# Kernel tuning notes

Measured on AMD Instinct MI355X. Metric: run time of the kernel, lower is better.

Reference implementation:

```python
import jax, jax.numpy as jnp
import numpy as np

N, F_DIM, H_DIM = 8192, 128, 128

def setup_inputs() -> dict:
    key = jax.random.key(0)
    ks = jax.random.split(key, 7)
    inp = {
        "input": jax.random.normal(ks[0], (N, F_DIM), dtype=jnp.float32),
        "wavelets": jax.random.normal(ks[1], (N, N), dtype=jnp.float32) / np.sqrt(N),
        "wavelets_inv": jax.random.normal(ks[2], (N, N), dtype=jnp.float32) / np.sqrt(N),
        # layer 1 params
        "W1": jax.random.uniform(ks[3], (F_DIM, H_DIM), dtype=jnp.float32,
                                 minval=-np.sqrt(6.0/(F_DIM+H_DIM)), maxval=np.sqrt(6.0/(F_DIM+H_DIM))),
        "f1": jax.random.uniform(ks[4], (N,), dtype=jnp.float32, minval=0.9, maxval=1.1),
        # layer 2 params
        "W2": jax.random.uniform(ks[5], (H_DIM, H_DIM), dtype=jnp.float32,
                                 minval=-np.sqrt(6.0/(H_DIM+H_DIM)), maxval=np.sqrt(6.0/(H_DIM+H_DIM))),
        "f2": jax.random.uniform(ks[6], (N,), dtype=jnp.float32, minval=0.9, maxval=1.1),
    }
    return inp

def _gwnn_layer(features, wavelets, wavelets_inv, W, filt):
    # torch: wavelets @ diag(filt) @ (wavelets_inv @ (features @ W))
    # diag(filt) matmul == column-wise scale of wavelets (broadcast elementwise)
    xw = features @ W                      # [N, out]
    spec = wavelets_inv @ xw               # [N, out] spectral-domain features
    spec = filt[:, None] * spec            # apply learnable diagonal filter
    return wavelets @ spec                 # [N, out]

def reference(input, wavelets, wavelets_inv, W1, f1, W2, f2):
    # eval mode: dropout is identity
    h1 = jax.nn.relu(_gwnn_layer(input, wavelets, wavelets_inv, W1, f1))
    out = _gwnn_layer(h1, wavelets, wavelets_inv, W2, f2)
    return out
```

## Files before the change

kernel.cpp:

```cpp
#include <hip/hip_runtime.h>
#include <hip/hip_bf16.h>
#include <stdint.h>


typedef __attribute__((ext_vector_type(4))) float f32x4;
typedef __attribute__((ext_vector_type(8))) short s16x8;
typedef __attribute__((ext_vector_type(4))) short s16x4;

#define DEVI static __device__ __forceinline__

DEVI short bf1(float x){ __bf16 h = (__bf16)x; return __builtin_bit_cast(short, h); }

DEVI s16x8 cvt8(f32x4 lo, f32x4 hi){
  s16x8 r;
#pragma unroll
  for (int i = 0; i < 4; ++i){ r[i] = bf1(lo[i]); r[4+i] = bf1(hi[i]); }
  return r;
}

DEVI void glds16(const void* g, void* l){
  __builtin_amdgcn_global_load_lds((const __attribute__((address_space(1))) void*)g,
                                   (__attribute__((address_space(3))) void*)l, 16, 0, 0);
}

template<int N> DEVI void waitvm(){
  if constexpr (N == 0)       asm volatile("s_waitcnt vmcnt(0)"  ::: "memory");
  else if constexpr (N == 5)  asm volatile("s_waitcnt vmcnt(5)"  ::: "memory");
  else if constexpr (N == 6)  asm volatile("s_waitcnt vmcnt(6)"  ::: "memory");
  else if constexpr (N == 12) asm volatile("s_waitcnt vmcnt(12)" ::: "memory");
  else if constexpr (N == 18) asm volatile("s_waitcnt vmcnt(18)" ::: "memory");
}

__global__ __launch_bounds__(256, 1) void gemm_big(
    const float* __restrict__ Ap, const short* __restrict__ Btp,
    float* __restrict__ Pp, int K, int M)
{
  constexpr int BM = 128, BK = 32;
  constexpr int ASZ = BM*BK*4;
  constexpr int BSZ = 128*BK*2;
  constexpr int TSZ = ASZ + BSZ;
  constexpr int NBUF = 6, PRE = 4;
  __shared__ uint8_t lds[NBUF*TSZ];

  const int tid  = threadIdx.x;
  const int lane = tid & 63;
  const int wv   = tid >> 6;
  const int la   = lane & 15;
  const int g4   = lane >> 4;
  const int bxl  = ((blockIdx.x & 7) << 3) + (blockIdx.x >> 3);
  const int m0   = bxl * BM;
  const int kq   = blockIdx.y;
  const int K4   = K >> 2;
  const int kb   = kq * K4;

  const float* gAbase = Ap + (size_t)m0*K + kb;
  int aoffg[4];
#pragma unroll
  for (int j = 0; j < 4; ++j){
    const int rl = (wv<<5) + (j<<3) + (lane>>3);
    aoffg[j] = rl*K + (((lane&7) ^ (rl&7))<<2);
  }

  const int nb0 = (wv<<5) + (lane>>2);
  const short* gB0 = Btp + (size_t)(nb0    )*K + kb + (((lane&3)^(nb0&3))<<3);
  const short* gB1 = Btp + (size_t)(nb0+16 )*K + kb + (((lane&3)^(nb0&3))<<3);

  int aoff[2][2];
#pragma unroll
  for (int mi = 0; mi < 2; ++mi){
    const int r = (wv<<5) + mi*16 + la;
#pragma unroll
    for (int p = 0; p < 2; ++p)
      aoff[mi][p] = r*128 + ((((g4<<1)+p)^(r&7))<<4);
  }
  int boff[8];
#pragma unroll
  for (int ni = 0; ni < 8; ++ni){
    const int n = ni*16 + la;
    boff[ni] = n*64 + ((g4^(n&3))<<4);
  }

  f32x4 acc[2][8] = {};

  int kk = 0;
  uint8_t* const lend = lds + NBUF*TSZ;
  uint8_t* bs = lds;
  uint8_t* bc = lds;

  auto STAGE = [&](){
    uint8_t* Ab = bs;
    uint8_t* Bb = bs + ASZ;
#pragma unroll
    for (int j = 0; j < 4; ++j)
      glds16(gAbase + aoffg[j] + kk, Ab + (wv<<12) + (j<<10));
    kk += BK;
    glds16(gB0, Bb + (wv<<11));
    glds16(gB1, Bb + (wv<<11) + 1024);
    gB0 += BK; gB1 += BK;
    bs += TSZ; if (bs == lend) bs = lds;
  };

  auto COMPUTE = [&](){
    const uint8_t* Ab = bc;
    const uint8_t* Bb = bc + ASZ;
    s16x8 a0 = cvt8(*(const f32x4*)(Ab + aoff[0][0]),
                    *(const f32x4*)(Ab + aoff[0][1]));
    s16x8 a1 = cvt8(*(const f32x4*)(Ab + aoff[1][0]),
                    *(const f32x4*)(Ab + aoff[1][1]));
#pragma unroll
    for (int ni = 0; ni < 8; ++ni){
      s16x8 b = *(const s16x8*)(Bb + boff[ni]);
      acc[0][ni] = __builtin_amdgcn_mfma_f32_16x16x32_bf16(a0, b, acc[0][ni], 0, 0, 0);
      acc[1][ni] = __builtin_amdgcn_mfma_f32_16x16x32_bf16(a1, b, acc[1][ni], 0, 0, 0);
    }
    bc += TSZ; if (bc == lend) bc = lds;
  };

  const int ns = K4 >> 5;
  for (int s = 0; s < PRE && s < ns; ++s) STAGE();

  for (int t = 0; t < ns; ++t){
    const int ahead = ns - 1 - t;
    if (ahead >= 3)      waitvm<18>();
    else if (ahead == 2) waitvm<12>();
    else if (ahead == 1) waitvm<6>();
    else                 waitvm<0>();
    __builtin_amdgcn_s_barrier();
    asm volatile("" ::: "memory");
    if (t + PRE < ns) STAGE();
    COMPUTE();
    asm volatile("" ::: "memory");
  }

  float* P = Pp + (size_t)kq * M * 128;
  const int rbase = m0 + (wv<<5) + (g4<<2);
#pragma unroll
  for (int mi = 0; mi < 2; ++mi)
#pragma unroll
    for (int ni = 0; ni < 8; ++ni)
#pragma unroll
      for (int r = 0; r < 4; ++r)
        P[(size_t)(rbase + mi*16 + r)*128 + ni*16 + la] = acc[mi][ni][r];
}

template<bool ABF>
__global__ __launch_bounds__(256, 1) void sgemm(
    const void* __restrict__ Ap, const short* __restrict__ Btp,
    void* __restrict__ Outp, int K, int M)
{
  constexpr int BM = 32, BN = 128, BK = 64;
  constexpr int ASZ = ABF ? BM*BK*2 : BM*BK*4;
  constexpr int BSZ = BN*BK*2;
  constexpr int TSZ = ASZ + BSZ;
  constexpr int NL  = ABF ? 5 : 6;
  constexpr int NBUF = 3, PRE = 2;
  __shared__ uint8_t lds[NBUF*TSZ];

  const int tid  = threadIdx.x;
  const int lane = tid & 63;
  const int wv   = tid >> 6;
  const int la   = lane & 15;
  const int g4   = lane >> 4;
  const int m0   = blockIdx.x * BM;

  const float* gA0 = nullptr; const float* gA1 = nullptr; const short* gAh = nullptr;
  if constexpr (!ABF){
    const float* Af = (const float*)Ap;
    int r0 = (wv<<3) + (lane>>4);
    int r1 = r0 + 4;
    gA0 = Af + (size_t)(m0+r0)*K + (((lane&15)^(r0&15))<<2);
    gA1 = Af + (size_t)(m0+r1)*K + (((lane&15)^(r1&15))<<2);
  } else {
    const short* Ah = (const short*)Ap;
    int r = (wv<<3) + (lane>>3);
    gAh = Ah + (size_t)(m0+r)*K + (((lane&7)^(r&7))<<3);
  }
  const int nb0 = (wv<<5) + (lane>>3);
  const short* gB0 = Btp + (size_t)(nb0    )*K + (((lane&7)^(nb0&7))<<3);
  const short* gB1 = Btp + (size_t)(nb0+ 8 )*K + (((lane&7)^(nb0&7))<<3);
  const short* gB2 = Btp + (size_t)(nb0+16 )*K + (((lane&7)^(nb0&7))<<3);
  const short* gB3 = Btp + (size_t)(nb0+24 )*K + (((lane&7)^(nb0&7))<<3);

  int aoff[2][2][2];
  int boff[2][2];
#pragma unroll
  for (int mi = 0; mi < 2; ++mi){
    const int r = mi*16 + la;
#pragma unroll
    for (int kf = 0; kf < 2; ++kf){
      if constexpr (!ABF){
        const int v0 = kf*8 + (g4<<1);
        aoff[mi][kf][0] = r*256 + (((v0  )^(r&15))<<4);
        aoff[mi][kf][1] = r*256 + (((v0+1)^(r&15))<<4);
      } else {
        const int u = kf*4 + g4;
        aoff[mi][kf][0] = r*128 + ((u^(r&7))<<4);
        aoff[mi][kf][1] = 0;
      }
    }
  }
#pragma unroll
  for (int ni = 0; ni < 2; ++ni){
    const int n = (wv<<5) + ni*16 + la;
#pragma unroll
    for (int kf = 0; kf < 2; ++kf){
      const int u = kf*4 + g4;
      boff[ni][kf] = n*128 + ((u^(n&7))<<4);
    }
  }

  f32x4 acc[2][2] = {};

  auto STAGE = [&](uint8_t* buf){
    uint8_t* Ab = buf;
    uint8_t* Bb = buf + ASZ;
    if constexpr (!ABF){
      glds16(gA0, Ab + (wv<<11));
      glds16(gA1, Ab + (wv<<11) + 1024);
      gA0 += BK; gA1 += BK;
    } else {
      glds16(gAh, Ab + (wv<<10));
      gAh += BK;
    }
    glds16(gB0, Bb + (wv<<12));
    glds16(gB1, Bb + (wv<<12) + 1024);
    glds16(gB2, Bb + (wv<<12) + 2048);
    glds16(gB3, Bb + (wv<<12) + 3072);
    gB0 += BK; gB1 += BK; gB2 += BK; gB3 += BK;
  };

  auto COMPUTE = [&](const uint8_t* buf){
    const uint8_t* Ab = buf;
    const uint8_t* Bb = buf + ASZ;
#pragma unroll
    for (int kf = 0; kf < 2; ++kf){
      s16x8 a0, a1, b0, b1;
      if constexpr (!ABF){
        a0 = cvt8(*(const f32x4*)(Ab + aoff[0][kf][0]), *(const f32x4*)(Ab + aoff[0][kf][1]));
        a1 = cvt8(*(const f32x4*)(Ab + aoff[1][kf][0]), *(const f32x4*)(Ab + aoff[1][kf][1]));
      } else {
        a0 = *(const s16x8*)(Ab + aoff[0][kf][0]);
        a1 = *(const s16x8*)(Ab + aoff[1][kf][0]);
      }
      b0 = *(const s16x8*)(Bb + boff[0][kf]);
      b1 = *(const s16x8*)(Bb + boff[1][kf]);
      acc[0][0] = __builtin_amdgcn_mfma_f32_16x16x32_bf16(a0, b0, acc[0][0], 0, 0, 0);
      acc[0][1] = __builtin_amdgcn_mfma_f32_16x16x32_bf16(a0, b1, acc[0][1], 0, 0, 0);
      acc[1][0] = __builtin_amdgcn_mfma_f32_16x16x32_bf16(a1, b0, acc[1][0], 0, 0, 0);
      acc[1][1] = __builtin_amdgcn_mfma_f32_16x16x32_bf16(a1, b1, acc[1][1], 0, 0, 0);
    }
  };

  const int ns = K >> 6;
  uint8_t* const lend = lds + NBUF*TSZ;
  uint8_t* bs = lds;
  uint8_t* bc = lds;
  for (int s = 0; s < PRE && s < ns; ++s){
    STAGE(bs);
    bs += TSZ; if (bs == lend) bs = lds;
  }
  for (int t = 0; t < ns; ++t){
    if (t < ns - 1) waitvm<NL>(); else waitvm<0>();
    __builtin_amdgcn_s_barrier();
    asm volatile("" ::: "memory");
    if (t + PRE < ns){
      STAGE(bs);
      bs += TSZ; if (bs == lend) bs = lds;
    }
    COMPUTE(bc);
    bc += TSZ; if (bc == lend) bc = lds;
    asm volatile("" ::: "memory");
  }

  const int mbase = m0 + (g4<<2);
  const int nc0   = (wv<<5) + la;
#pragma unroll
  for (int mi = 0; mi < 2; ++mi){
#pragma unroll
    for (int ni = 0; ni < 2; ++ni){
      s16x4 pk;
#pragma unroll
      for (int r = 0; r < 4; ++r) pk[r] = bf1(acc[mi][ni][r]);
      *(s16x4*)((short*)Outp + (size_t)(nc0 + (ni<<4))*M + (mbase + (mi<<4))) = pk;
    }
  }
}


__global__ __launch_bounds__(256) void red_t(
    const float* __restrict__ Pp, const float* __restrict__ fp,
    short* __restrict__ out, int M)
{
  __shared__ short t[128*65];
  const size_t S = (size_t)M*128;
  const int m0 = blockIdx.x * 64;
  const int tid = threadIdx.x;
#pragma unroll
  for (int it = 0; it < 8; ++it){
    const int idx = it*256 + tid;
    const int m = idx >> 5, nq = idx & 31;
    const float* base = Pp + (size_t)(m0+m)*128;
    f32x4 a = ((const f32x4*)(base      ))[nq];
    f32x4 b = ((const f32x4*)(base +   S))[nq];
    f32x4 c = ((const f32x4*)(base + 2*S))[nq];
    f32x4 d = ((const f32x4*)(base + 3*S))[nq];
    const float fv = fp[m0+m];
#pragma unroll
    for (int j = 0; j < 4; ++j)
      t[(nq*4+j)*65 + m] = bf1(fv * ((a[j] + b[j]) + (c[j] + d[j])));
  }
  __syncthreads();
#pragma unroll
  for (int it = 0; it < 8; ++it){
    const int idx = it*256 + tid;
    const int n = idx >> 4, mc = idx & 15;
    s16x4 v;
#pragma unroll
    for (int j = 0; j < 4; ++j) v[j] = t[n*65 + mc*4 + j];
    *(s16x4*)(out + (size_t)n*M + m0 + mc*4) = v;
  }
}

__global__ __launch_bounds__(256) void red_r(
    const float* __restrict__ Pp, short* __restrict__ out, int M)
{
  const size_t S = (size_t)M*128;
  const size_t i0 = (size_t)(blockIdx.x*256 + threadIdx.x) * 8;
  s16x8 v;
#pragma unroll
  for (int h = 0; h < 2; ++h){
    f32x4 a = *(const f32x4*)(Pp + i0 + 4*h);
    f32x4 b = *(const f32x4*)(Pp + i0 + 4*h + S);
    f32x4 c = *(const f32x4*)(Pp + i0 + 4*h + 2*S);
    f32x4 d = *(const f32x4*)(Pp + i0 + 4*h + 3*S);
#pragma unroll
    for (int j = 0; j < 4; ++j)
      v[4*h+j] = bf1(fmaxf((a[j] + b[j]) + (c[j] + d[j]), 0.0f));
  }
  *(s16x8*)(out + i0) = v;
}

__global__ __launch_bounds__(256) void red_f(
    const float* __restrict__ Pp, float* __restrict__ out, int M)
{
  const size_t S = (size_t)M*128;
  const size_t i0 = (size_t)(blockIdx.x*256 + threadIdx.x) * 4;
  f32x4 a = *(const f32x4*)(Pp + i0);
  f32x4 b = *(const f32x4*)(Pp + i0 + S);
  f32x4 c = *(const f32x4*)(Pp + i0 + 2*S);
  f32x4 d = *(const f32x4*)(Pp + i0 + 3*S);
  *(f32x4*)(out + i0) = (a + b) + (c + d);
}

__global__ void wtrans_k(const float* __restrict__ W1, const float* __restrict__ W2,
                         short* __restrict__ T1, short* __restrict__ T2){
  const int idx = blockIdx.x*256 + threadIdx.x;
  const int m = idx >> 14, rem = idx & 16383;
  const int n = rem >> 7, k = rem & 127;
  const float* W = m ? W2 : W1;
  short* T = m ? T2 : T1;
  T[n*128 + k] = bf1(W[k*128 + n]);
}

extern "C" void kernel_launch(void* const* d_in, const int* in_sizes, int n_in,
                              void* d_out, int out_size, void* d_ws, size_t ws_size,
                              hipStream_t stream){
  const float* input = (const float*)d_in[0];
  const float* wav   = (const float*)d_in[1];
  const float* winv  = (const float*)d_in[2];
  const float* W1    = (const float*)d_in[3];
  const float* f1    = (const float*)d_in[4];
  const float* W2    = (const float*)d_in[5];
  const float* f2    = (const float*)d_in[6];

  constexpr int M = 8192;
  uint8_t* ws = (uint8_t*)d_ws;
  short* W1T = (short*)(ws);
  short* W2T = (short*)(ws + (32<<10));
  short* XWT = (short*)(ws + (64<<10));
  short* SPT = (short*)(ws + (64<<10) + (2<<20));
  short* H1  = (short*)(ws + (64<<10) + (4<<20));
  float* P   = (float*)(ws + (64<<10) + (6<<20));

  dim3 b(256);
  dim3 gbig(M/128, 4);
  dim3 gns(M/32);
  dim3 grt(M/64);
  dim3 grr(M*128/(256*8));
  dim3 grf(M*128/(256*4));
  dim3 gt(128);

  wtrans_k<<<gt, b, 0, stream>>>(W1, W2, W1T, W2T);
  sgemm<false><<<gns, b, 0, stream>>>(input, W1T, XWT, 128, M);
  gemm_big<<<gbig, b, 0, stream>>>(winv, XWT, P, M, M);
  red_t  <<<grt, b, 0, stream>>>(P, f1, SPT, M);
  gemm_big<<<gbig, b, 0, stream>>>(wav, SPT, P, M, M);
  red_r  <<<grr, b, 0, stream>>>(P, H1, M);
  sgemm<true ><<<gns, b, 0, stream>>>(H1, W2T, XWT, 128, M);
  gemm_big<<<gbig, b, 0, stream>>>(winv, XWT, P, M, M);
  red_t  <<<grt, b, 0, stream>>>(P, f2, SPT, M);
  gemm_big<<<gbig, b, 0, stream>>>(wav, SPT, P, M, M);
  red_f  <<<grf, b, 0, stream>>>(P, (float*)d_out, M);
}
```

Before: 299.2 us.

## Double big-GEMM row tile to 256 and split K eightfold

The main N×N GEMM now uses 256-row tiles (4 m-subtiles per wave), so each loaded B tile feeds twice as many MFMAs. To keep the grid size, K is split 8 ways instead of 4, and the reduction kernels now sum 8 partial buffers. The LDS pipeline shrinks from 6 buffers to 3 with prefetch depth 2 to fit the larger tile. The costs are twice the partial-sum traffic in the reduction kernels and more accumulator registers, and the shallower prefetch may expose more memory latency.

```diff
diff --git a/kernel.cpp b/kernel.cpp
--- a/kernel.cpp
+++ b/kernel.cpp
@@ -27,19 +27,18 @@
   if constexpr (N == 0)       asm volatile("s_waitcnt vmcnt(0)"  ::: "memory");
   else if constexpr (N == 5)  asm volatile("s_waitcnt vmcnt(5)"  ::: "memory");
   else if constexpr (N == 6)  asm volatile("s_waitcnt vmcnt(6)"  ::: "memory");
-  else if constexpr (N == 12) asm volatile("s_waitcnt vmcnt(12)" ::: "memory");
-  else if constexpr (N == 18) asm volatile("s_waitcnt vmcnt(18)" ::: "memory");
+  else if constexpr (N == 10) asm volatile("s_waitcnt vmcnt(10)" ::: "memory");
 }
 
 __global__ __launch_bounds__(256, 1) void gemm_big(
     const float* __restrict__ Ap, const short* __restrict__ Btp,
     float* __restrict__ Pp, int K, int M)
 {
-  constexpr int BM = 128, BK = 32;
+  constexpr int BM = 256, BK = 32;
   constexpr int ASZ = BM*BK*4;
   constexpr int BSZ = 128*BK*2;
   constexpr int TSZ = ASZ + BSZ;
-  constexpr int NBUF = 6, PRE = 4;
+  constexpr int NBUF = 3, PRE = 2;
   __shared__ uint8_t lds[NBUF*TSZ];
 
   const int tid  = threadIdx.x;
@@ -47,17 +46,17 @@
   const int wv   = tid >> 6;
   const int la   = lane & 15;
   const int g4   = lane >> 4;
-  const int bxl  = ((blockIdx.x & 7) << 3) + (blockIdx.x >> 3);
+  const int bxl  = ((blockIdx.x & 7) << 2) + (blockIdx.x >> 3);
   const int m0   = bxl * BM;
   const int kq   = blockIdx.y;
-  const int K4   = K >> 2;
-  const int kb   = kq * K4;
+  const int K8   = K >> 3;
+  const int kb   = kq * K8;
 
   const float* gAbase = Ap + (size_t)m0*K + kb;
-  int aoffg[4];
-#pragma unroll
-  for (int j = 0; j < 4; ++j){
-    const int rl = (wv<<5) + (j<<3) + (lane>>3);
+  int aoffg[8];
+#pragma unroll
+  for (int j = 0; j < 8; ++j){
+    const int rl = (wv<<6) + (j<<3) + (lane>>3);
     aoffg[j] = rl*K + (((lane&7) ^ (rl&7))<<2);
   }
 
@@ -65,22 +64,22 @@
   const short* gB0 = Btp + (size_t)(nb0    )*K + kb + (((lane&3)^(nb0&3))<<3);
   const short* gB1 = Btp + (size_t)(nb0+16 )*K + kb + (((lane&3)^(nb0&3))<<3);
 
-  int aoff[2][2];
-#pragma unroll
-  for (int mi = 0; mi < 2; ++mi){
-    const int r = (wv<<5) + mi*16 + la;
+  int aoff[4][2];
+#pragma unroll
+  for (int mi = 0; mi < 4; ++mi){
+    const int r = (wv<<6) + mi*16 + la;
 #pragma unroll
     for (int p = 0; p < 2; ++p)
-      aoff[mi][p] = r*128 + ((((g4<<1)+p)^(r&7))<<4);
+      aoff[mi][p] = r*128 + ((((g4<<1)+p) ^ (r&7))<<4);
   }
   int boff[8];
 #pragma unroll
   for (int ni = 0; ni < 8; ++ni){
     const int n = ni*16 + la;
-    boff[ni] = n*64 + ((g4^(n&3))<<4);
-  }
-
-  f32x4 acc[2][8] = {};
+    boff[ni] = n*64 + ((g4 ^ (n&3))<<4);
+  }
+
+  f32x4 acc[4][8] = {};
 
   int kk = 0;
   uint8_t* const lend = lds + NBUF*TSZ;
@@ -91,40 +90,39 @@
     uint8_t* Ab = bs;
     uint8_t* Bb = bs + ASZ;
 #pragma unroll
-    for (int j = 0; j < 4; ++j)
-      glds16(gAbase + aoffg[j] + kk, Ab + (wv<<12) + (j<<10));
-    kk += BK;
+    for (int j = 0; j < 8; ++j)
+      glds16(gAbase + aoffg[j] + kk, Ab + (wv<<13) + (j<<10));
     glds16(gB0, Bb + (wv<<11));
     glds16(gB1, Bb + (wv<<11) + 1024);
     gB0 += BK; gB1 += BK;
+    kk += BK;
     bs += TSZ; if (bs == lend) bs = lds;
   };
 
   auto COMPUTE = [&](){
     const uint8_t* Ab = bc;
     const uint8_t* Bb = bc + ASZ;
-    s16x8 a0 = cvt8(*(const f32x4*)(Ab + aoff[0][0]),
-                    *(const f32x4*)(Ab + aoff[0][1]));
-    s16x8 a1 = cvt8(*(const f32x4*)(Ab + aoff[1][0]),
-                    *(const f32x4*)(Ab + aoff[1][1]));
+    s16x8 a0 = cvt8(*(const f32x4*)(Ab + aoff[0][0]), *(const f32x4*)(Ab + aoff[0][1]));
+    s16x8 a1 = cvt8(*(const f32x4*)(Ab + aoff[1][0]), *(const f32x4*)(Ab + aoff[1][1]));
+    s16x8 a2 = cvt8(*(const f32x4*)(Ab + aoff[2][0]), *(const f32x4*)(Ab + aoff[2][1]));
+    s16x8 a3 = cvt8(*(const f32x4*)(Ab + aoff[3][0]), *(const f32x4*)(Ab + aoff[3][1]));
 #pragma unroll
     for (int ni = 0; ni < 8; ++ni){
       s16x8 b = *(const s16x8*)(Bb + boff[ni]);
       acc[0][ni] = __builtin_amdgcn_mfma_f32_16x16x32_bf16(a0, b, acc[0][ni], 0, 0, 0);
       acc[1][ni] = __builtin_amdgcn_mfma_f32_16x16x32_bf16(a1, b, acc[1][ni], 0, 0, 0);
+      acc[2][ni] = __builtin_amdgcn_mfma_f32_16x16x32_bf16(a2, b, acc[2][ni], 0, 0, 0);
+      acc[3][ni] = __builtin_amdgcn_mfma_f32_16x16x32_bf16(a3, b, acc[3][ni], 0, 0, 0);
     }
     bc += TSZ; if (bc == lend) bc = lds;
   };
 
-  const int ns = K4 >> 5;
+  const int ns = K8 >> 5;
   for (int s = 0; s < PRE && s < ns; ++s) STAGE();
 
   for (int t = 0; t < ns; ++t){
-    const int ahead = ns - 1 - t;
-    if (ahead >= 3)      waitvm<18>();
-    else if (ahead == 2) waitvm<12>();
-    else if (ahead == 1) waitvm<6>();
-    else                 waitvm<0>();
+    if (t < ns - 1) waitvm<10>();
+    else            waitvm<0>();
     __builtin_amdgcn_s_barrier();
     asm volatile("" ::: "memory");
     if (t + PRE < ns) STAGE();
@@ -133,9 +131,9 @@
   }
 
   float* P = Pp + (size_t)kq * M * 128;
-  const int rbase = m0 + (wv<<5) + (g4<<2);
-#pragma unroll
-  for (int mi = 0; mi < 2; ++mi)
+  const int rbase = m0 + (wv<<6) + (g4<<2);
+#pragma unroll
+  for (int mi = 0; mi < 4; ++mi)
 #pragma unroll
     for (int ni = 0; ni < 8; ++ni)
 #pragma unroll
@@ -287,6 +285,14 @@
 }
 
 
+DEVI f32x4 sum8(const float* p, size_t S){
+  f32x4 v = (*(const f32x4*)(p)       + *(const f32x4*)(p +   S))
+          + (*(const f32x4*)(p + 2*S) + *(const f32x4*)(p + 3*S));
+  f32x4 w = (*(const f32x4*)(p + 4*S) + *(const f32x4*)(p + 5*S))
+          + (*(const f32x4*)(p + 6*S) + *(const f32x4*)(p + 7*S));
+  return v + w;
+}
+
 __global__ __launch_bounds__(256) void red_t(
     const float* __restrict__ Pp, const float* __restrict__ fp,
     short* __restrict__ out, int M)
@@ -299,15 +305,11 @@
   for (int it = 0; it < 8; ++it){
     const int idx = it*256 + tid;
     const int m = idx >> 5, nq = idx & 31;
-    const float* base = Pp + (size_t)(m0+m)*128;
-    f32x4 a = ((const f32x4*)(base      ))[nq];
-    f32x4 b = ((const f32x4*)(base +   S))[nq];
-    f32x4 c = ((const f32x4*)(base + 2*S))[nq];
-    f32x4 d = ((const f32x4*)(base + 3*S))[nq];
+    f32x4 v = sum8(Pp + (size_t)(m0+m)*128 + nq*4, S);
     const float fv = fp[m0+m];
 #pragma unroll
     for (int j = 0; j < 4; ++j)
-      t[(nq*4+j)*65 + m] = bf1(fv * ((a[j] + b[j]) + (c[j] + d[j])));
+      t[(nq*4+j)*65 + m] = bf1(fv * v[j]);
   }
   __syncthreads();
 #pragma unroll
@@ -329,13 +331,10 @@
   s16x8 v;
 #pragma unroll
   for (int h = 0; h < 2; ++h){
-    f32x4 a = *(const f32x4*)(Pp + i0 + 4*h);
-    f32x4 b = *(const f32x4*)(Pp + i0 + 4*h + S);
-    f32x4 c = *(const f32x4*)(Pp + i0 + 4*h + 2*S);
-    f32x4 d = *(const f32x4*)(Pp + i0 + 4*h + 3*S);
+    f32x4 a = sum8(Pp + i0 + 4*h, S);
 #pragma unroll
     for (int j = 0; j < 4; ++j)
-      v[4*h+j] = bf1(fmaxf((a[j] + b[j]) + (c[j] + d[j]), 0.0f));
+      v[4*h+j] = bf1(fmaxf(a[j], 0.0f));
   }
   *(s16x8*)(out + i0) = v;
 }
@@ -345,11 +344,7 @@
 {
   const size_t S = (size_t)M*128;
   const size_t i0 = (size_t)(blockIdx.x*256 + threadIdx.x) * 4;
-  f32x4 a = *(const f32x4*)(Pp + i0);
-  f32x4 b = *(const f32x4*)(Pp + i0 + S);
-  f32x4 c = *(const f32x4*)(Pp + i0 + 2*S);
-  f32x4 d = *(const f32x4*)(Pp + i0 + 3*S);
-  *(f32x4*)(out + i0) = (a + b) + (c + d);
+  *(f32x4*)(out + i0) = sum8(Pp + i0, S);
 }
 
 __global__ void wtrans_k(const float* __restrict__ W1, const float* __restrict__ W2,
@@ -383,7 +378,7 @@
   float* P   = (float*)(ws + (64<<10) + (6<<20));
 
   dim3 b(256);
-  dim3 gbig(M/128, 4);
+  dim3 gbig(M/256, 8);
   dim3 gns(M/32);
   dim3 grt(M/64);
   dim3 grr(M*128/(256*8));
```

Result: slower. 339.5 us (+13.5%).
